# Performance work log

Hardware: AMD Instinct MI355X
Metric: run time of the kernel (lower is better)

## Reference

```python
import jax, jax.numpy as jnp
import numpy as np

LN_EPS = 1e-5

def _next_fast_len(n):
    # smallest 5-smooth integer >= n (matches scipy.fftpack.next_fast_len)
    while True:
        m = n
        for p in (2, 3, 5):
            while m % p == 0:
                m //= p
        if m == 1:
            return n
        n += 1

def _conv1d_fft(x, w):
    # x: (b, h, N, d), convolved along axis -2 against w: (h, M) along axis -1.
    # Matches the torch reference: multiply by conj(rfft(w)), roll by -1, take last N.
    N = x.shape[-2]
    M = w.shape[-1]
    L = _next_fast_len(N + M - 1)
    fx = jnp.fft.rfft(x, n=L, axis=-2)                    # (b, h, F, d) complex
    fw = jnp.fft.rfft(w, n=L, axis=-1)                    # (h, F) complex
    out = jnp.fft.irfft(fx * jnp.conj(fw)[..., None], L, axis=-2)
    out = jnp.roll(out, -1, axis=-2)
    return out[..., L - N:, :]                            # (b, h, N, d)

def setup_inputs() -> dict:
    key = jax.random.key(0)
    ks = jax.random.split(key, 5)
    b, n, d, h = 4, 4096, 1024, 8
    dh = d // h
    s = 0.02
    return {
        "x": jax.random.normal(ks[0], (b, n, d), jnp.float32),
        "ln_gamma": jnp.ones((d,), jnp.float32),
        "ln_beta": jnp.zeros((d,), jnp.float32),
        "w_in": jax.random.normal(ks[1], (d, d), jnp.float32) * s,
        "b_in": jnp.zeros((d,), jnp.float32),
        "initial_state": jax.random.normal(ks[2], (h, dh), jnp.float32),
        "alpha": jax.random.normal(ks[3], (h,), jnp.float32),
        "w_out": jax.random.normal(ks[4], (d, d), jnp.float32) * s,
        "b_out": jnp.zeros((d,), jnp.float32),
    }

def reference(x, ln_gamma, ln_beta, w_in, b_in, initial_state, alpha, w_out, b_out):
    b, n, d = x.shape
    h, dh = initial_state.shape
    # LayerNorm
    mu = jnp.mean(x, axis=-1, keepdims=True)
    var = jnp.mean((x - mu) ** 2, axis=-1, keepdims=True)
    xn = (x - mu) * jax.lax.rsqrt(var + LN_EPS) * ln_gamma + ln_beta
    # project_in (torch Linear: y = x @ W.T + b)
    xp = xn @ w_in.T + b_in
    # b n (h d) -> b h n d
    xh = xp.reshape(b, n, h, dh).transpose(0, 2, 1, 3)
    # prepend learned initial state, then first difference along n
    init = jnp.broadcast_to(initial_state[None, :, None, :], (b, h, 1, dh))
    xc = jnp.concatenate([init, xh], axis=2)
    xd = xc[:, :, 1:] - xc[:, :, :-1]                     # (b, h, n, dh)
    # EMA weights per head
    a = jax.nn.sigmoid(alpha)[:, None]                    # (h, 1)
    ar = jnp.arange(n)
    w = a * (1.0 - a) ** ar[::-1]                         # (h, n)
    out = _conv1d_fft(xd, w)
    # initial-state contribution
    init_w = (1.0 - a) ** (ar + 1)                        # (h, n)
    out = out + init_w[:, :, None] * initial_state[:, None, :]
    # b h n d -> b n (h d), then project_out
    out = out.transpose(0, 2, 1, 3).reshape(b, n, d)
    return out @ w_out.T + b_out
```

## Files before the change

kernel.cpp:

```cpp
#include <hip/hip_runtime.h>
#include <stdint.h>

typedef float  f32x4 __attribute__((ext_vector_type(4)));
typedef __bf16 bf16x8 __attribute__((ext_vector_type(8)));
typedef short  s16x8 __attribute__((ext_vector_type(8)));
typedef unsigned short u16;

static __device__ __forceinline__ u16 f2bf(float f) {
  unsigned u = __float_as_uint(f);
  u += 0x7fffu + ((u >> 16) & 1u);
  return (u16)(u >> 16);
}
static __device__ __forceinline__ float bf2f(u16 u) {
  return __uint_as_float(((unsigned)u) << 16);
}

static __device__ __forceinline__ void async_copy16(void* lds, const void* g) {
  __builtin_amdgcn_global_load_lds(
      (const __attribute__((address_space(1))) unsigned int*)g,
      (__attribute__((address_space(3))) unsigned int*)lds, 16, 0, 0);
}

__global__ __launch_bounds__(256) void cvt_k(const float* __restrict__ in,
                                             u16* __restrict__ out, int n4) {
  int i = blockIdx.x * 256 + threadIdx.x;
  if (i >= n4) return;
  float4 v = reinterpret_cast<const float4*>(in)[i];
  ushort4 o;
  o.x = f2bf(v.x); o.y = f2bf(v.y); o.z = f2bf(v.z); o.w = f2bf(v.w);
  reinterpret_cast<ushort4*>(out)[i] = o;
}

__global__ __launch_bounds__(256) void ln_k(const float* __restrict__ x,
                                            const float* __restrict__ g,
                                            const float* __restrict__ b,
                                            u16* __restrict__ xn) {
  const int D = 1024;
  const int row = blockIdx.x;
  const int tid = threadIdx.x;
  const float4 v = reinterpret_cast<const float4*>(x + (size_t)row * D)[tid];
  float s  = v.x + v.y + v.z + v.w;
  float s2 = v.x * v.x + v.y * v.y + v.z * v.z + v.w * v.w;
  #pragma unroll
  for (int off = 32; off > 0; off >>= 1) {
    s  += __shfl_down(s, off);
    s2 += __shfl_down(s2, off);
  }
  __shared__ float red[8];
  const int lane = tid & 63, wv = tid >> 6;
  if (lane == 0) { red[wv] = s; red[4 + wv] = s2; }
  __syncthreads();
  s  = red[0] + red[1] + red[2] + red[3];
  s2 = red[4] + red[5] + red[6] + red[7];
  const float mu   = s * (1.0f / D);
  const float var  = s2 * (1.0f / D) - mu * mu;
  const float rstd = rsqrtf(var + 1e-5f);
  const float4 gv = reinterpret_cast<const float4*>(g)[tid];
  const float4 bv = reinterpret_cast<const float4*>(b)[tid];
  ushort4 o;
  o.x = f2bf((v.x - mu) * rstd * gv.x + bv.x);
  o.y = f2bf((v.y - mu) * rstd * gv.y + bv.y);
  o.z = f2bf((v.z - mu) * rstd * gv.z + bv.z);
  o.w = f2bf((v.w - mu) * rstd * gv.w + bv.w);
  reinterpret_cast<ushort4*>(xn + (size_t)row * D)[tid] = o;
}

static __device__ __forceinline__ s16x8 ldfrag(const u16* b, int row, int ks,
                                               int fkc, int sx) {
  return *reinterpret_cast<const s16x8*>(
      &b[row * 64 + ((((ks << 2) + fkc) ^ sx) << 3)]);
}

template<int OUT_BF16>
__global__ __launch_bounds__(512, 2) void gemm8_k(const u16* __restrict__ A,
                                                  const u16* __restrict__ Bm,
                                                  const float* __restrict__ bias,
                                                  void* __restrict__ Cv,
                                                  int M, int N, int K) {
  const int tid  = threadIdx.x;
  const int lane = tid & 63;
  const int wv   = tid >> 6;
  const int wrr  = wv >> 2;
  const int wcc  = wv & 3;
  const int ntN  = N >> 8;
  const int nwg  = (M >> 8) * ntN;
  const int bid  = blockIdx.x;
  const int wgid = (bid & 7) * (nwg >> 3) + (bid >> 3);
  const int mt = wgid / ntN, nt = wgid % ntN;
  const int m0 = mt << 8, n0 = nt << 8;

  __shared__ __align__(16) u16 sA[2][256 * 64];
  __shared__ __align__(16) u16 sB[2][256 * 64];

  const int trow = tid >> 3;
  const int tch  = tid & 7;
  const int csw  = (tch ^ (trow & 7)) << 3;
  const u16* gA = A  + (size_t)(m0 + trow) * K + csw;
  const u16* gB = Bm + (size_t)(n0 + trow) * K + csw;
  const int lofs = trow * 64 + (tch << 3);

  f32x4 acc[8][4];
  #pragma unroll
  for (int i = 0; i < 8; ++i)
    #pragma unroll
    for (int j = 0; j < 4; ++j) acc[i][j] = f32x4{0.f, 0.f, 0.f, 0.f};

  const int fr  = lane & 15;
  const int fkc = lane >> 4;
  const int sx  = fr & 7;
  const int abase = wrr << 7;
  const int bbase = wcc << 6;

  const int NK = K >> 6;

  #pragma unroll
  for (int r = 0; r < 4; ++r) {
    async_copy16(&sA[0][lofs + r * 4096], gA + (size_t)r * 64 * K);
    async_copy16(&sB[0][lofs + r * 4096], gB + (size_t)r * 64 * K);
  }
  asm volatile("s_waitcnt vmcnt(0)" ::: "memory");
  __builtin_amdgcn_s_barrier();

  s16x8 af[4][2], bfr[2][2];

  for (int kt = 0; kt < NK; ++kt) {
    const int cur = kt & 1;
    const u16* bA = sA[cur];
    const u16* bB = sB[cur];
    u16* nA = sA[cur ^ 1];
    u16* nB = sB[cur ^ 1];
    const bool pf = (kt + 1 < NK);
    const size_t ko = (size_t)(kt + 1) << 6;

    #pragma unroll
    for (int i = 0; i < 4; ++i)
      #pragma unroll
      for (int ks = 0; ks < 2; ++ks)
        af[i][ks] = ldfrag(bA, abase + i * 16 + fr, ks, fkc, sx);
    #pragma unroll
    for (int j = 0; j < 2; ++j)
      #pragma unroll
      for (int ks = 0; ks < 2; ++ks)
        bfr[j][ks] = ldfrag(bB, bbase + j * 16 + fr, ks, fkc, sx);
    if (pf) {
      async_copy16(&nA[lofs], gA + ko);
      async_copy16(&nA[lofs + 4096], gA + ko + (size_t)64 * K);
    }
    __builtin_amdgcn_s_barrier();
    __builtin_amdgcn_s_setprio(1);
    #pragma unroll
    for (int i = 0; i < 4; ++i)
      #pragma unroll
      for (int j = 0; j < 2; ++j)
        #pragma unroll
        for (int ks = 0; ks < 2; ++ks)
          acc[i][j] = __builtin_amdgcn_mfma_f32_16x16x32_bf16(
              __builtin_bit_cast(bf16x8, af[i][ks]),
              __builtin_bit_cast(bf16x8, bfr[j][ks]), acc[i][j], 0, 0, 0);
    __builtin_amdgcn_s_setprio(0);
    __builtin_amdgcn_s_barrier();

    #pragma unroll
    for (int j = 0; j < 2; ++j)
      #pragma unroll
      for (int ks = 0; ks < 2; ++ks)
        bfr[j][ks] = ldfrag(bB, bbase + 32 + j * 16 + fr, ks, fkc, sx);
    if (pf) {
      async_copy16(&nA[lofs + 2 * 4096], gA + ko + (size_t)128 * K);
      async_copy16(&nA[lofs + 3 * 4096], gA + ko + (size_t)192 * K);
    }
    __builtin_amdgcn_s_barrier();
    __builtin_amdgcn_s_setprio(1);
    #pragma unroll
    for (int i = 0; i < 4; ++i)
      #pragma unroll
      for (int j = 0; j < 2; ++j)
        #pragma unroll
        for (int ks = 0; ks < 2; ++ks)
          acc[i][2 + j] = __builtin_amdgcn_mfma_f32_16x16x32_bf16(
              __builtin_bit_cast(bf16x8, af[i][ks]),
              __builtin_bit_cast(bf16x8, bfr[j][ks]), acc[i][2 + j], 0, 0, 0);
    __builtin_amdgcn_s_setprio(0);
    __builtin_amdgcn_s_barrier();

    #pragma unroll
    for (int i = 0; i < 4; ++i)
      #pragma unroll
      for (int ks = 0; ks < 2; ++ks)
        af[i][ks] = ldfrag(bA, abase + 64 + i * 16 + fr, ks, fkc, sx);
    if (pf) {
      async_copy16(&nB[lofs], gB + ko);
      async_copy16(&nB[lofs + 4096], gB + ko + (size_t)64 * K);
    }
    __builtin_amdgcn_s_barrier();
    __builtin_amdgcn_s_setprio(1);
    #pragma unroll
    for (int i = 0; i < 4; ++i)
      #pragma unroll
      for (int j = 0; j < 2; ++j)
        #pragma unroll
        for (int ks = 0; ks < 2; ++ks)
          acc[4 + i][2 + j] = __builtin_amdgcn_mfma_f32_16x16x32_bf16(
              __builtin_bit_cast(bf16x8, af[i][ks]),
              __builtin_bit_cast(bf16x8, bfr[j][ks]), acc[4 + i][2 + j], 0, 0, 0);
    __builtin_amdgcn_s_setprio(0);
    __builtin_amdgcn_s_barrier();

    #pragma unroll
    for (int j = 0; j < 2; ++j)
      #pragma unroll
      for (int ks = 0; ks < 2; ++ks)
        bfr[j][ks] = ldfrag(bB, bbase + j * 16 + fr, ks, fkc, sx);
    if (pf) {
      async_copy16(&nB[lofs + 2 * 4096], gB + ko + (size_t)128 * K);
      async_copy16(&nB[lofs + 3 * 4096], gB + ko + (size_t)192 * K);
    }
    __builtin_amdgcn_s_barrier();
    __builtin_amdgcn_s_setprio(1);
    #pragma unroll
    for (int i = 0; i < 4; ++i)
      #pragma unroll
      for (int j = 0; j < 2; ++j)
        #pragma unroll
        for (int ks = 0; ks < 2; ++ks)
          acc[4 + i][j] = __builtin_amdgcn_mfma_f32_16x16x32_bf16(
              __builtin_bit_cast(bf16x8, af[i][ks]),
              __builtin_bit_cast(bf16x8, bfr[j][ks]), acc[4 + i][j], 0, 0, 0);
    __builtin_amdgcn_s_setprio(0);
    if (pf) asm volatile("s_waitcnt vmcnt(0)" ::: "memory");
    __builtin_amdgcn_s_barrier();
  }

  const int cr = (lane >> 4) << 2;
  const int cc = lane & 15;
  #pragma unroll
  for (int nj = 0; nj < 4; ++nj) {
    const int col = n0 + (wcc << 6) + nj * 16 + cc;
    const float bv = bias[col];
    #pragma unroll
    for (int mi = 0; mi < 8; ++mi) {
      #pragma unroll
      for (int rr = 0; rr < 4; ++rr) {
        const int row = m0 + (wrr << 7) + mi * 16 + cr + rr;
        const float val = acc[mi][nj][rr] + bv;
        if (OUT_BF16) ((u16*)Cv)[(size_t)row * N + col] = f2bf(val);
        else          ((float*)Cv)[(size_t)row * N + col] = val;
      }
    }
  }
}

__global__ __launch_bounds__(256) void ema_chunk_k(const u16* __restrict__ xp,
                                                   const float* __restrict__ alpha,
                                                   const float* __restrict__ init,
                                                   float* __restrict__ carry) {
  const int Nn = 4096, Dd = 1024, T = 128, nCh = 32;
  int bid = blockIdx.x;
  const int cg = bid & 1;  bid >>= 1;
  const int q  = bid & 31; bid >>= 5;
  const int bb = bid;
  const int c = cg * 512 + threadIdx.x * 2;
  const int h = c >> 7;
  const float a = 1.0f / (1.0f + __expf(-alpha[h]));
  const float r = 1.0f - a;
  const u16* px = xp + ((size_t)bb * Nn + (size_t)q * T) * Dd + c;
  float p0, p1;
  if (q == 0) { p0 = init[c]; p1 = init[c + 1]; }
  else { ushort2 pv = *(const ushort2*)(px - Dd); p0 = bf2f(pv.x); p1 = bf2f(pv.y); }
  float L0 = 0.f, L1 = 0.f;
  #pragma unroll 4
  for (int t = 0; t < T; ++t) {
    ushort2 v = *(const ushort2*)(px + (size_t)t * Dd);
    float v0 = bf2f(v.x), v1 = bf2f(v.y);
    L0 = r * L0 + a * (v0 - p0);
    L1 = r * L1 + a * (v1 - p1);
    p0 = v0; p1 = v1;
  }
  *(float2*)(carry + ((size_t)bb * nCh + q) * Dd + c) = make_float2(L0, L1);
}

__global__ __launch_bounds__(256) void ema_carry_k(const float* __restrict__ alpha,
                                                   const float* __restrict__ init,
                                                   float* __restrict__ carry) {
  const int Dd = 1024, nCh = 32;
  const int idx = blockIdx.x * 256 + threadIdx.x;
  const int c  = idx & (Dd - 1);
  const int bb = idx >> 10;
  const int h = c >> 7;
  const float a = 1.0f / (1.0f + __expf(-alpha[h]));
  const float r = 1.0f - a;
  float rT = r;
  #pragma unroll
  for (int s = 0; s < 7; ++s) rT *= rT;
  float L[32];
  #pragma unroll
  for (int q = 0; q < nCh; ++q)
    L[q] = carry[((size_t)bb * nCh + q) * Dd + c];
  float cin = init[c];
  #pragma unroll
  for (int q = 0; q < nCh; ++q) {
    carry[((size_t)bb * nCh + q) * Dd + c] = cin;
    cin = rT * cin + L[q];
  }
}

__global__ __launch_bounds__(256) void ema_apply_k(const u16* __restrict__ xp,
                                                   const float* __restrict__ alpha,
                                                   const float* __restrict__ init,
                                                   const float* __restrict__ carry,
                                                   u16* __restrict__ ob) {
  const int Nn = 4096, Dd = 1024, T = 128, nCh = 32;
  int bid = blockIdx.x;
  const int cg = bid & 1;  bid >>= 1;
  const int q  = bid & 31; bid >>= 5;
  const int bb = bid;
  const int c = cg * 512 + threadIdx.x * 2;
  const int h = c >> 7;
  const float a = 1.0f / (1.0f + __expf(-alpha[h]));
  const float r = 1.0f - a;
  const u16* px = xp + ((size_t)bb * Nn + (size_t)q * T) * Dd + c;
  u16* po = ob + ((size_t)bb * Nn + (size_t)q * T) * Dd + c;
  float2 Oin = *(const float2*)(carry + ((size_t)bb * nCh + q) * Dd + c);
  float O0 = Oin.x, O1 = Oin.y;
  float p0, p1;
  if (q == 0) { p0 = init[c]; p1 = init[c + 1]; }
  else { ushort2 pv = *(const ushort2*)(px - Dd); p0 = bf2f(pv.x); p1 = bf2f(pv.y); }
  #pragma unroll 4
  for (int t = 0; t < T; ++t) {
    ushort2 v = *(const ushort2*)(px + (size_t)t * Dd);
    float v0 = bf2f(v.x), v1 = bf2f(v.y);
    O0 = r * O0 + a * (v0 - p0);
    O1 = r * O1 + a * (v1 - p1);
    p0 = v0; p1 = v1;
    ushort2 o; o.x = f2bf(O0); o.y = f2bf(O1);
    *(ushort2*)(po + (size_t)t * Dd) = o;
  }
}

extern "C" void kernel_launch(void* const* d_in, const int* in_sizes, int n_in,
                              void* d_out, int out_size, void* d_ws, size_t ws_size,
                              hipStream_t stream) {
  const float* x     = (const float*)d_in[0];
  const float* ln_g  = (const float*)d_in[1];
  const float* ln_b  = (const float*)d_in[2];
  const float* w_in  = (const float*)d_in[3];
  const float* b_in  = (const float*)d_in[4];
  const float* init  = (const float*)d_in[5];
  const float* alpha = (const float*)d_in[6];
  const float* w_out = (const float*)d_in[7];
  const float* b_out = (const float*)d_in[8];
  float* out = (float*)d_out;

  const int B = 4, N = 4096, D = 1024;
  const int M = B * N;

  char* p = (char*)d_ws;
  u16*   xn  = (u16*)p; p += (size_t)M * D * sizeof(u16);
  u16*   wi  = (u16*)p; p += (size_t)D * D * sizeof(u16);
  u16*   wo  = (u16*)p; p += (size_t)D * D * sizeof(u16);
  u16*   xpb = (u16*)p; p += (size_t)M * D * sizeof(u16);
  float* cr  = (float*)p; p += (size_t)B * 32 * D * sizeof(float);
  u16*   ob  = (u16*)p;

  const int n4 = D * D / 4;
  cvt_k<<<dim3((n4 + 255) / 256), dim3(256), 0, stream>>>(w_in, wi, n4);
  cvt_k<<<dim3((n4 + 255) / 256), dim3(256), 0, stream>>>(w_out, wo, n4);
  ln_k<<<dim3(M), dim3(256), 0, stream>>>(x, ln_g, ln_b, xn);
  gemm8_k<1><<<dim3((M / 256) * (D / 256)), dim3(512), 0, stream>>>(xn, wi, b_in, xpb, M, D, D);
  ema_chunk_k<<<dim3(B * 32 * 2), dim3(256), 0, stream>>>(xpb, alpha, init, cr);
  ema_carry_k<<<dim3(B * D / 256), dim3(256), 0, stream>>>(alpha, init, cr);
  ema_apply_k<<<dim3(B * 32 * 2), dim3(256), 0, stream>>>(xpb, alpha, init, cr, ob);
  gemm8_k<0><<<dim3((M / 256) * (D / 256)), dim3(512), 0, stream>>>(ob, wo, b_out, out, M, D, D);
}
```

Measured before the change: 153.8 us.

## Fuse EMA chunk scan into GEMM epilogue and restage GEMM loads

The in-projection GEMM now stages its output tile through LDS, writes coalesced vectorized rows, and computes the per-chunk EMA partial sums from that tile in the epilogue. This removes the separate ema_chunk kernel and its second read of xp. The carry kernel now patches in the boundary term that crosses chunks, reading the first and last rows of each chunk. The GEMM load schedule is also reworked: all eight async copies are issued at once with partial vmcnt waits, and the LDS row mapping is permuted. The costs are a serial 128-step scan per column inside the epilogue and extra barriers.

```diff
diff --git a/kernel.cpp b/kernel.cpp
--- a/kernel.cpp
+++ b/kernel.cpp
@@ -71,11 +71,13 @@
       &b[row * 64 + ((((ks << 2) + fkc) ^ sx) << 3)]);
 }
 
-template<int OUT_BF16>
+template<int MODE>
 __global__ __launch_bounds__(512, 2) void gemm8_k(const u16* __restrict__ A,
                                                   const u16* __restrict__ Bm,
                                                   const float* __restrict__ bias,
                                                   void* __restrict__ Cv,
+                                                  const float* __restrict__ alpha,
+                                                  float* __restrict__ Lp,
                                                   int M, int N, int K) {
   const int tid  = threadIdx.x;
   const int lane = tid & 63;
@@ -89,15 +91,22 @@
   const int mt = wgid / ntN, nt = wgid % ntN;
   const int m0 = mt << 8, n0 = nt << 8;
 
-  __shared__ __align__(16) u16 sA[2][256 * 64];
-  __shared__ __align__(16) u16 sB[2][256 * 64];
-
-  const int trow = tid >> 3;
-  const int tch  = tid & 7;
-  const int csw  = (tch ^ (trow & 7)) << 3;
-  const u16* gA = A  + (size_t)(m0 + trow) * K + csw;
-  const u16* gB = Bm + (size_t)(n0 + trow) * K + csw;
-  const int lofs = trow * 64 + (tch << 3);
+  __shared__ __align__(16) u16 smem[4 * 16384];
+
+  const int u   = tid >> 3;
+  const int tch = tid & 7;
+  const int csw = (tch ^ (u & 7)) << 3;
+  const int ldst = u * 64 + (tch << 3);
+  constexpr int amap[4] = {0, 2, 1, 3};
+  const u16* gAr[4];
+  const u16* gBr[4];
+  #pragma unroll
+  for (int r = 0; r < 4; ++r) {
+    gAr[r] = A + (size_t)(m0 + amap[r] * 64 + u) * K + csw;
+    const int l = r * 64 + u;
+    const int grow = ((l >> 5) & 3) * 64 + (l >> 7) * 32 + (l & 31);
+    gBr[r] = Bm + (size_t)(n0 + grow) * K + csw;
+  }
 
   f32x4 acc[8][4];
   #pragma unroll
@@ -108,27 +117,31 @@
   const int fr  = lane & 15;
   const int fkc = lane >> 4;
   const int sx  = fr & 7;
-  const int abase = wrr << 7;
-  const int bbase = wcc << 6;
 
   const int NK = K >> 6;
 
-  #pragma unroll
-  for (int r = 0; r < 4; ++r) {
-    async_copy16(&sA[0][lofs + r * 4096], gA + (size_t)r * 64 * K);
-    async_copy16(&sB[0][lofs + r * 4096], gB + (size_t)r * 64 * K);
-  }
-  asm volatile("s_waitcnt vmcnt(0)" ::: "memory");
+#define ISSUE8(nA, nB, koff)                                      \
+  async_copy16(&(nA)[ldst],            gAr[0] + (koff));          \
+  async_copy16(&(nA)[ldst + 4096],     gAr[1] + (koff));          \
+  async_copy16(&(nB)[ldst],            gBr[0] + (koff));          \
+  async_copy16(&(nB)[ldst + 4096],     gBr[1] + (koff));          \
+  async_copy16(&(nB)[ldst + 2 * 4096], gBr[2] + (koff));          \
+  async_copy16(&(nB)[ldst + 3 * 4096], gBr[3] + (koff));          \
+  async_copy16(&(nA)[ldst + 2 * 4096], gAr[2] + (koff));          \
+  async_copy16(&(nA)[ldst + 3 * 4096], gAr[3] + (koff));
+
+  { u16* nA = smem; u16* nB = smem + 32768; ISSUE8(nA, nB, 0) }
+  asm volatile("s_waitcnt vmcnt(4)" ::: "memory");
   __builtin_amdgcn_s_barrier();
 
   s16x8 af[4][2], bfr[2][2];
 
   for (int kt = 0; kt < NK; ++kt) {
     const int cur = kt & 1;
-    const u16* bA = sA[cur];
-    const u16* bB = sB[cur];
-    u16* nA = sA[cur ^ 1];
-    u16* nB = sB[cur ^ 1];
+    const u16* bA = smem + cur * 16384;
+    const u16* bB = smem + 32768 + cur * 16384;
+    u16* nA = (u16*)(smem + (cur ^ 1) * 16384);
+    u16* nB = (u16*)(smem + 32768 + (cur ^ 1) * 16384);
     const bool pf = (kt + 1 < NK);
     const size_t ko = (size_t)(kt + 1) << 6;
 
@@ -136,16 +149,13 @@
     for (int i = 0; i < 4; ++i)
       #pragma unroll
       for (int ks = 0; ks < 2; ++ks)
-        af[i][ks] = ldfrag(bA, abase + i * 16 + fr, ks, fkc, sx);
+        af[i][ks] = ldfrag(bA, wrr * 64 + i * 16 + fr, ks, fkc, sx);
     #pragma unroll
     for (int j = 0; j < 2; ++j)
       #pragma unroll
       for (int ks = 0; ks < 2; ++ks)
-        bfr[j][ks] = ldfrag(bB, bbase + j * 16 + fr, ks, fkc, sx);
-    if (pf) {
-      async_copy16(&nA[lofs], gA + ko);
-      async_copy16(&nA[lofs + 4096], gA + ko + (size_t)64 * K);
-    }
+        bfr[j][ks] = ldfrag(bB, wcc * 32 + j * 16 + fr, ks, fkc, sx);
+    if (pf) { ISSUE8(nA, nB, ko) }
     __builtin_amdgcn_s_barrier();
     __builtin_amdgcn_s_setprio(1);
     #pragma unroll
@@ -158,17 +168,15 @@
               __builtin_bit_cast(bf16x8, af[i][ks]),
               __builtin_bit_cast(bf16x8, bfr[j][ks]), acc[i][j], 0, 0, 0);
     __builtin_amdgcn_s_setprio(0);
+    if (pf) asm volatile("s_waitcnt vmcnt(10)" ::: "memory");
+    else    asm volatile("s_waitcnt vmcnt(2)" ::: "memory");
     __builtin_amdgcn_s_barrier();
 
     #pragma unroll
     for (int j = 0; j < 2; ++j)
       #pragma unroll
       for (int ks = 0; ks < 2; ++ks)
-        bfr[j][ks] = ldfrag(bB, bbase + 32 + j * 16 + fr, ks, fkc, sx);
-    if (pf) {
-      async_copy16(&nA[lofs + 2 * 4096], gA + ko + (size_t)128 * K);
-      async_copy16(&nA[lofs + 3 * 4096], gA + ko + (size_t)192 * K);
-    }
+        bfr[j][ks] = ldfrag(bB, 128 + wcc * 32 + j * 16 + fr, ks, fkc, sx);
     __builtin_amdgcn_s_barrier();
     __builtin_amdgcn_s_setprio(1);
     #pragma unroll
@@ -181,17 +189,15 @@
               __builtin_bit_cast(bf16x8, af[i][ks]),
               __builtin_bit_cast(bf16x8, bfr[j][ks]), acc[i][2 + j], 0, 0, 0);
     __builtin_amdgcn_s_setprio(0);
+    if (pf) asm volatile("s_waitcnt vmcnt(8)" ::: "memory");
+    else    asm volatile("s_waitcnt vmcnt(0)" ::: "memory");
     __builtin_amdgcn_s_barrier();
 
     #pragma unroll
     for (int i = 0; i < 4; ++i)
       #pragma unroll
       for (int ks = 0; ks < 2; ++ks)
-        af[i][ks] = ldfrag(bA, abase + 64 + i * 16 + fr, ks, fkc, sx);
-    if (pf) {
-      async_copy16(&nB[lofs], gB + ko);
-      async_copy16(&nB[lofs + 4096], gB + ko + (size_t)64 * K);
-    }
+        af[i][ks] = ldfrag(bA, 128 + wrr * 64 + i * 16 + fr, ks, fkc, sx);
     __builtin_amdgcn_s_barrier();
     __builtin_amdgcn_s_setprio(1);
     #pragma unroll
@@ -210,11 +216,7 @@
     for (int j = 0; j < 2; ++j)
       #pragma unroll
       for (int ks = 0; ks < 2; ++ks)
-        bfr[j][ks] = ldfrag(bB, bbase + j * 16 + fr, ks, fkc, sx);
-    if (pf) {
-      async_copy16(&nB[lofs + 2 * 4096], gB + ko + (size_t)128 * K);
-      async_copy16(&nB[lofs + 3 * 4096], gB + ko + (size_t)192 * K);
-    }
+        bfr[j][ks] = ldfrag(bB, wcc * 32 + j * 16 + fr, ks, fkc, sx);
     __builtin_amdgcn_s_barrier();
     __builtin_amdgcn_s_setprio(1);
     #pragma unroll
@@ -227,59 +229,87 @@
               __builtin_bit_cast(bf16x8, af[i][ks]),
               __builtin_bit_cast(bf16x8, bfr[j][ks]), acc[4 + i][j], 0, 0, 0);
     __builtin_amdgcn_s_setprio(0);
-    if (pf) asm volatile("s_waitcnt vmcnt(0)" ::: "memory");
-    __builtin_amdgcn_s_barrier();
-  }
-
+    asm volatile("s_waitcnt vmcnt(4)" ::: "memory");
+    __builtin_amdgcn_s_barrier();
+  }
+#undef ISSUE8
+
+  float* sC = (float*)smem;
   const int cr = (lane >> 4) << 2;
   const int cc = lane & 15;
-  #pragma unroll
-  for (int nj = 0; nj < 4; ++nj) {
-    const int col = n0 + (wcc << 6) + nj * 16 + cc;
-    const float bv = bias[col];
-    #pragma unroll
-    for (int mi = 0; mi < 8; ++mi) {
-      #pragma unroll
-      for (int rr = 0; rr < 4; ++rr) {
-        const int row = m0 + (wrr << 7) + mi * 16 + cr + rr;
-        const float val = acc[mi][nj][rr] + bv;
-        if (OUT_BF16) ((u16*)Cv)[(size_t)row * N + col] = f2bf(val);
-        else          ((float*)Cv)[(size_t)row * N + col] = val;
+  float bv[4];
+  #pragma unroll
+  for (int nj = 0; nj < 4; ++nj) bv[nj] = bias[n0 + wcc * 64 + nj * 16 + cc];
+
+  #pragma unroll
+  for (int p = 0; p < 2; ++p) {
+    __syncthreads();
+    if (wrr == p) {
+      #pragma unroll
+      for (int mi = 0; mi < 8; ++mi)
+        #pragma unroll
+        for (int nj = 0; nj < 4; ++nj)
+          #pragma unroll
+          for (int rr = 0; rr < 4; ++rr) {
+            const int row = mi * 16 + cr + rr;
+            const int col = wcc * 64 + nj * 16 + cc;
+            sC[row * 256 + (col ^ ((row & 4) << 2))] = acc[mi][nj][rr] + bv[nj];
+          }
+    }
+    __syncthreads();
+    #pragma unroll 4
+    for (int it = 0; it < 16; ++it) {
+      const int row  = it * 8 + wv;
+      const int col0 = (tid & 63) * 4;
+      f32x4 v = *(const f32x4*)&sC[row * 256 + (col0 ^ ((row & 4) << 2))];
+      const size_t goff = (size_t)(m0 + p * 128 + row) * N + n0 + col0;
+      if (MODE == 1) {
+        ushort4 o; o.x = f2bf(v[0]); o.y = f2bf(v[1]); o.z = f2bf(v[2]); o.w = f2bf(v[3]);
+        *(ushort4*)&((u16*)Cv)[goff] = o;
+      } else {
+        *(f32x4*)&((float*)Cv)[goff] = v;
       }
     }
-  }
-}
-
-__global__ __launch_bounds__(256) void ema_chunk_k(const u16* __restrict__ xp,
+    if (MODE == 1 && tid < 256) {
+      const int col = tid;
+      const int hh = (n0 + col) >> 7;
+      const float a = 1.0f / (1.0f + __expf(-alpha[hh]));
+      const float rw = 1.0f - a;
+      float prev = sC[col];
+      float L = 0.f;
+      int t = 1;
+      for (; t + 8 <= 128; t += 8) {
+        float w0 = sC[(t+0)*256 + (col ^ (((t+0)&4)<<2))];
+        float w1 = sC[(t+1)*256 + (col ^ (((t+1)&4)<<2))];
+        float w2 = sC[(t+2)*256 + (col ^ (((t+2)&4)<<2))];
+        float w3 = sC[(t+3)*256 + (col ^ (((t+3)&4)<<2))];
+        float w4 = sC[(t+4)*256 + (col ^ (((t+4)&4)<<2))];
+        float w5 = sC[(t+5)*256 + (col ^ (((t+5)&4)<<2))];
+        float w6 = sC[(t+6)*256 + (col ^ (((t+6)&4)<<2))];
+        float w7 = sC[(t+7)*256 + (col ^ (((t+7)&4)<<2))];
+        L = rw * L + a * (w0 - prev);
+        L = rw * L + a * (w1 - w0);
+        L = rw * L + a * (w2 - w1);
+        L = rw * L + a * (w3 - w2);
+        L = rw * L + a * (w4 - w3);
+        L = rw * L + a * (w5 - w4);
+        L = rw * L + a * (w6 - w5);
+        L = rw * L + a * (w7 - w6);
+        prev = w7;
+      }
+      for (; t < 128; ++t) {
+        float w = sC[t*256 + (col ^ ((t&4)<<2))];
+        L = rw * L + a * (w - prev); prev = w;
+      }
+      const int bb = m0 >> 12;
+      const int q  = ((m0 >> 7) & 31) + p;
+      Lp[((size_t)bb * 32 + q) * 1024 + n0 + col] = L;
+    }
+  }
+}
+
+__global__ __launch_bounds__(256) void ema_carry_k(const u16* __restrict__ xpb,
                                                    const float* __restrict__ alpha,
-                                                   const float* __restrict__ init,
-                                                   float* __restrict__ carry) {
-  const int Nn = 4096, Dd = 1024, T = 128, nCh = 32;
-  int bid = blockIdx.x;
-  const int cg = bid & 1;  bid >>= 1;
-  const int q  = bid & 31; bid >>= 5;
-  const int bb = bid;
-  const int c = cg * 512 + threadIdx.x * 2;
-  const int h = c >> 7;
-  const float a = 1.0f / (1.0f + __expf(-alpha[h]));
-  const float r = 1.0f - a;
-  const u16* px = xp + ((size_t)bb * Nn + (size_t)q * T) * Dd + c;
-  float p0, p1;
-  if (q == 0) { p0 = init[c]; p1 = init[c + 1]; }
-  else { ushort2 pv = *(const ushort2*)(px - Dd); p0 = bf2f(pv.x); p1 = bf2f(pv.y); }
-  float L0 = 0.f, L1 = 0.f;
-  #pragma unroll 4
-  for (int t = 0; t < T; ++t) {
-    ushort2 v = *(const ushort2*)(px + (size_t)t * Dd);
-    float v0 = bf2f(v.x), v1 = bf2f(v.y);
-    L0 = r * L0 + a * (v0 - p0);
-    L1 = r * L1 + a * (v1 - p1);
-    p0 = v0; p1 = v1;
-  }
-  *(float2*)(carry + ((size_t)bb * nCh + q) * Dd + c) = make_float2(L0, L1);
-}
-
-__global__ __launch_bounds__(256) void ema_carry_k(const float* __restrict__ alpha,
                                                    const float* __restrict__ init,
                                                    float* __restrict__ carry) {
   const int Dd = 1024, nCh = 32;
@@ -289,18 +319,20 @@
   const int h = c >> 7;
   const float a = 1.0f / (1.0f + __expf(-alpha[h]));
   const float r = 1.0f - a;
-  float rT = r;
-  #pragma unroll
-  for (int s = 0; s < 7; ++s) rT *= rT;
-  float L[32];
-  #pragma unroll
-  for (int q = 0; q < nCh; ++q)
-    L[q] = carry[((size_t)bb * nCh + q) * Dd + c];
+  float q_ = r, r127 = 1.0f;
+  #pragma unroll
+  for (int s = 0; s < 7; ++s) { r127 *= q_; q_ *= q_; }
+  const float rT = r127 * r;
   float cin = init[c];
-  #pragma unroll
+  float prevv = cin;
   for (int q = 0; q < nCh; ++q) {
-    carry[((size_t)bb * nCh + q) * Dd + c] = cin;
-    cin = rT * cin + L[q];
+    const size_t rowb = (size_t)bb * 4096 + (size_t)q * 128;
+    const float v0 = bf2f(xpb[rowb * Dd + c]);
+    const size_t off = ((size_t)bb * nCh + q) * Dd + c;
+    const float L = carry[off] + a * r127 * (v0 - prevv);
+    carry[off] = cin;
+    cin = rT * cin + L;
+    prevv = bf2f(xpb[(rowb + 127) * Dd + c]);
   }
 }
 
@@ -366,9 +398,10 @@
   cvt_k<<<dim3((n4 + 255) / 256), dim3(256), 0, stream>>>(w_in, wi, n4);
   cvt_k<<<dim3((n4 + 255) / 256), dim3(256), 0, stream>>>(w_out, wo, n4);
   ln_k<<<dim3(M), dim3(256), 0, stream>>>(x, ln_g, ln_b, xn);
-  gemm8_k<1><<<dim3((M / 256) * (D / 256)), dim3(512), 0, stream>>>(xn, wi, b_in, xpb, M, D, D);
-  ema_chunk_k<<<dim3(B * 32 * 2), dim3(256), 0, stream>>>(xpb, alpha, init, cr);
-  ema_carry_k<<<dim3(B * D / 256), dim3(256), 0, stream>>>(alpha, init, cr);
+  gemm8_k<1><<<dim3((M / 256) * (D / 256)), dim3(512), 0, stream>>>(
+      xn, wi, b_in, xpb, alpha, cr, M, D, D);
+  ema_carry_k<<<dim3(B * D / 256), dim3(256), 0, stream>>>(xpb, alpha, init, cr);
   ema_apply_k<<<dim3(B * 32 * 2), dim3(256), 0, stream>>>(xpb, alpha, init, cr, ob);
-  gemm8_k<0><<<dim3((M / 256) * (D / 256)), dim3(512), 0, stream>>>(ob, wo, b_out, out, M, D, D);
-}
+  gemm8_k<0><<<dim3((M / 256) * (D / 256)), dim3(512), 0, stream>>>(
+      ob, wo, b_out, out, nullptr, nullptr, M, D, D);
+}
```

Result: slower. 161.1 us (+4.7%).
